# Optimization experiments

Hardware: AMD Instinct MI355X
Metric: run time of the kernel (lower is better)

The kernel has to match this reference:

```python
import jax, jax.numpy as jnp
import numpy as np

MIN_NORM = 1e-15
C = 1.0  # c_in == c_out == 1.0  (K = 1/c)
N, D = 16384, 64


def _expmap0(u, c):
    # exp map at origin of the hyperboloid; u has first coord 0 (tangent at origin)
    sqrtK = (1.0 / c) ** 0.5
    x = u[..., 1:]
    xn = jnp.maximum(jnp.linalg.norm(x, axis=-1, keepdims=True), MIN_NORM)
    theta = xn / sqrtK
    return jnp.concatenate([sqrtK * jnp.cosh(theta), sqrtK * jnp.sinh(theta) * x / xn], axis=-1)


def _logmap0(x, c):
    sqrtK = (1.0 / c) ** 0.5
    y = x[..., 1:]
    yn = jnp.maximum(jnp.linalg.norm(y, axis=-1, keepdims=True), MIN_NORM)
    theta = jnp.maximum(x[..., :1] / sqrtK, 1.0 + 1e-7)
    return jnp.concatenate([jnp.zeros_like(theta), sqrtK * jnp.arccosh(theta) * y / yn], axis=-1)


def _proj(x, c):
    # re-project onto the hyperboloid: recompute the time coordinate
    K = 1.0 / c
    y = x[..., 1:]
    first = jnp.sqrt(jnp.maximum(K + jnp.sum(y * y, axis=-1, keepdims=True), MIN_NORM))
    return jnp.concatenate([first, y], axis=-1)


def setup_inputs():
    key = jax.random.key(0)
    k1, k2, k3 = jax.random.split(key, 3)
    # valid hyperboloid points: expmap0 of tangent vectors (first coord 0)
    tang = 0.5 * jax.random.normal(k1, (N, D - 1), dtype=jnp.float32)
    x = _expmap0(jnp.concatenate([jnp.zeros((N, 1), jnp.float32), tang], axis=-1), C)
    # sparse-ish row-normalized adjacency (avg degree ~32), stored dense
    a = jax.random.uniform(k2, (N, N), dtype=jnp.float32)
    mask = (a > 1.0 - 32.0 / N).astype(jnp.float32)
    adj = mask / jnp.maximum(mask.sum(axis=-1, keepdims=True), 1.0)
    W = (jax.random.normal(k3, (D, D), dtype=jnp.float32) / np.float32(np.sqrt(D)))
    return {"x": x, "adj": adj, "W": W}


def reference(x, adj, W):
    # LorentzLinear (no bias, dropout=0): mobius_matvec = expmap0(logmap0(x) @ W^T)
    u = _logmap0(x, C)                       # [N, D], u[:, 0] == 0
    h = _proj(_expmap0(u @ W.T, C), C)
    # LorentzAgg (no attention): aggregate neighbors in tangent space at origin
    ht = _logmap0(h, C)                      # [N, D]
    h = _proj(_expmap0(adj @ ht, C), C)      # [N, D]
    # LorentzAct: apply act in tangent space at origin, proj_tan0, re-project
    xt = jax.nn.relu(_logmap0(h, C))
    xt = xt * jnp.concatenate([jnp.zeros((1,), xt.dtype), jnp.ones((D - 1,), xt.dtype)])  # proj_tan0
    return _proj(_expmap0(xt, C), C)
```

## Files before the change

### kernel.cpp

```cpp
#include <hip/hip_runtime.h>
#include <math.h>

#define NROWS 16384
#define MINN 1e-15f

typedef float vf4 __attribute__((ext_vector_type(4)));

__device__ __forceinline__ float waveSum(float v) {
    #pragma unroll
    for (int m = 32; m >= 1; m >>= 1) v += __shfl_xor(v, m, 64);
    return v;
}

__global__ __launch_bounds__(256) void prep_kernel(
    const float* __restrict__ x, const float* __restrict__ W,
    float* __restrict__ ht)
{
    __shared__ float WT[64 * 64];
    for (int t = threadIdx.x; t < 64 * 64; t += 256) {
        int k = t >> 6, d = t & 63;
        WT[d * 64 + k] = W[t];
    }
    __syncthreads();
    const int lane = threadIdx.x & 63;
    const int row = blockIdx.x * 4 + (threadIdx.x >> 6);

    float xv = x[row * 64 + lane];
    float sq = (lane == 0) ? 0.f : xv * xv;
    float yn = fmaxf(sqrtf(waveSum(sq)), MINN);
    float theta = fmaxf(__shfl(xv, 0, 64), 1.0f + 1e-7f);
    float s = acoshf(theta) / yn;
    float u = (lane == 0) ? 0.f : s * xv;

    float h1 = 0.f;
    #pragma unroll
    for (int d = 1; d < 64; ++d)
        h1 = fmaf(__shfl(u, d, 64), WT[d * 64 + lane], h1);

    float z = (lane == 0) ? 0.f : h1;
    float zn = fmaxf(sqrtf(waveSum(z * z)), MINN);
    float sh = sinhf(zn);
    float ey = sh * z / zn;
    float s2 = waveSum(ey * ey);
    float first = sqrtf(fmaxf(1.f + s2, MINN));
    float ynb = fmaxf(sqrtf(s2), MINN);
    float th2 = fmaxf(first, 1.0f + 1e-7f);
    float coef = acoshf(th2) / ynb;
    float htv = (lane == 0) ? 0.f : coef * ey;
    ht[row * 64 + lane] = htv;
}

__global__ __launch_bounds__(256) void agg_kernel(
    const float* __restrict__ adj, const float* __restrict__ ht,
    float* __restrict__ out)
{
    const int lane = threadIdx.x & 63;
    const int row = blockIdx.x * 4 + (threadIdx.x >> 6);
    const float* arow = adj + (size_t)row * NROWS;

    float acc = 0.f;
    for (int it = 0; it < NROWS / 1024; ++it) {
        const float* base = arow + it * 1024 + lane * 4;
        vf4 v0 = __builtin_nontemporal_load((const vf4*)(base + 0));
        vf4 v1 = __builtin_nontemporal_load((const vf4*)(base + 256));
        vf4 v2 = __builtin_nontemporal_load((const vf4*)(base + 512));
        vf4 v3 = __builtin_nontemporal_load((const vf4*)(base + 768));
        #pragma unroll
        for (int w = 0; w < 4; ++w) {
            vf4 v = (w == 0) ? v0 : (w == 1) ? v1 : (w == 2) ? v2 : v3;
            unsigned int any = __float_as_uint(v.x) | __float_as_uint(v.y) |
                               __float_as_uint(v.z) | __float_as_uint(v.w);
            unsigned long long mask = __ballot(any != 0u);
            int jwin = it * 1024 + w * 256;
            while (mask) {
                int L = __ffsll((long long)mask) - 1;
                mask &= mask - 1;
                float a0 = __shfl(v.x, L, 64);
                float a1 = __shfl(v.y, L, 64);
                float a2 = __shfl(v.z, L, 64);
                float a3 = __shfl(v.w, L, 64);
                int jbase = jwin + L * 4;
                if (a0 != 0.f) acc = fmaf(a0, ht[(size_t)(jbase + 0) * 64 + lane], acc);
                if (a1 != 0.f) acc = fmaf(a1, ht[(size_t)(jbase + 1) * 64 + lane], acc);
                if (a2 != 0.f) acc = fmaf(a2, ht[(size_t)(jbase + 2) * 64 + lane], acc);
                if (a3 != 0.f) acc = fmaf(a3, ht[(size_t)(jbase + 3) * 64 + lane], acc);
            }
        }
    }

    float z = (lane == 0) ? 0.f : acc;
    float zn = fmaxf(sqrtf(waveSum(z * z)), MINN);
    float sh = sinhf(zn);
    float ey = sh * z / zn;
    float s2 = waveSum(ey * ey);
    float first = sqrtf(fmaxf(1.f + s2, MINN));
    float ynb = fmaxf(sqrtf(s2), MINN);
    float th2 = fmaxf(first, 1.0f + 1e-7f);
    float l = acoshf(th2) / ynb * ey;
    float xt = fmaxf(l, 0.f);
    if (lane == 0) xt = 0.f;
    float xn = fmaxf(sqrtf(waveSum(xt * xt)), MINN);
    float sh2 = sinhf(xn);
    float oy = sh2 * xt / xn;
    float o0 = sqrtf(fmaxf(1.f + waveSum(oy * oy), MINN));
    float outv = (lane == 0) ? o0 : oy;
    out[row * 64 + lane] = outv;
}

extern "C" void kernel_launch(void* const* d_in, const int* in_sizes, int n_in,
                              void* d_out, int out_size, void* d_ws, size_t ws_size,
                              hipStream_t stream) {
    const float* x   = (const float*)d_in[0];
    const float* adj = (const float*)d_in[1];
    const float* W   = (const float*)d_in[2];
    float* out = (float*)d_out;
    float* ht  = (float*)d_ws;

    prep_kernel<<<NROWS / 4, 256, 0, stream>>>(x, W, ht);
    agg_kernel<<<NROWS / 4, 256, 0, stream>>>(adj, ht, out);
}
```

Baseline: 1.344 ms.

## Fuse prep into aggregation by recomputing neighbor ht on the fly

Merges the two kernels into one. Each wave now recomputes the tangent vector (logmap, a 64x64 matvec from shared memory, expmap, proj, logmap) for every nonzero neighbor instead of reading a precomputed ht buffer. It also double-buffers the adjacency loads by prefetching the next 1024-column chunk. This removes a kernel launch and the ht round trip through memory, but it redoes the per-row transform about 32 times per row (the average degree), adding a lot of ALU and shuffle work inside a serial loop.

Result: slower. 1.980 ms (+47.3%).

```diff
diff --git a/kernel.cpp b/kernel.cpp
--- a/kernel.cpp
+++ b/kernel.cpp
@@ -3,6 +3,7 @@
 
 #define NROWS 16384
 #define MINN 1e-15f
+#define NITER (NROWS / 1024)
 
 typedef float vf4 __attribute__((ext_vector_type(4)));
 
@@ -12,20 +13,10 @@
     return v;
 }
 
-__global__ __launch_bounds__(256) void prep_kernel(
-    const float* __restrict__ x, const float* __restrict__ W,
-    float* __restrict__ ht)
+__device__ __forceinline__ float compute_ht(
+    const float* __restrict__ x, const float* WT, int j, int lane)
 {
-    __shared__ float WT[64 * 64];
-    for (int t = threadIdx.x; t < 64 * 64; t += 256) {
-        int k = t >> 6, d = t & 63;
-        WT[d * 64 + k] = W[t];
-    }
-    __syncthreads();
-    const int lane = threadIdx.x & 63;
-    const int row = blockIdx.x * 4 + (threadIdx.x >> 6);
-
-    float xv = x[row * 64 + lane];
+    float xv = x[(size_t)j * 64 + lane];
     float sq = (lane == 0) ? 0.f : xv * xv;
     float yn = fmaxf(sqrtf(waveSum(sq)), MINN);
     float theta = fmaxf(__shfl(xv, 0, 64), 1.0f + 1e-7f);
@@ -46,28 +37,44 @@
     float ynb = fmaxf(sqrtf(s2), MINN);
     float th2 = fmaxf(first, 1.0f + 1e-7f);
     float coef = acoshf(th2) / ynb;
-    float htv = (lane == 0) ? 0.f : coef * ey;
-    ht[row * 64 + lane] = htv;
+    return (lane == 0) ? 0.f : coef * ey;
 }
 
-__global__ __launch_bounds__(256) void agg_kernel(
-    const float* __restrict__ adj, const float* __restrict__ ht,
-    float* __restrict__ out)
+__global__ __launch_bounds__(256) void fused_kernel(
+    const float* __restrict__ x, const float* __restrict__ adj,
+    const float* __restrict__ W, float* __restrict__ out)
 {
     const int lane = threadIdx.x & 63;
     const int row = blockIdx.x * 4 + (threadIdx.x >> 6);
     const float* arow = adj + (size_t)row * NROWS;
 
+    const float* b0 = arow + lane * 4;
+    vf4 c0 = __builtin_nontemporal_load((const vf4*)(b0 + 0));
+    vf4 c1 = __builtin_nontemporal_load((const vf4*)(b0 + 256));
+    vf4 c2 = __builtin_nontemporal_load((const vf4*)(b0 + 512));
+    vf4 c3 = __builtin_nontemporal_load((const vf4*)(b0 + 768));
+
+    __shared__ float WT[64 * 64];
+    for (int t = threadIdx.x; t < 64 * 64; t += 256) {
+        int k = t >> 6, d = t & 63;
+        WT[d * 64 + k] = W[t];
+    }
+    __syncthreads();
+
     float acc = 0.f;
-    for (int it = 0; it < NROWS / 1024; ++it) {
-        const float* base = arow + it * 1024 + lane * 4;
-        vf4 v0 = __builtin_nontemporal_load((const vf4*)(base + 0));
-        vf4 v1 = __builtin_nontemporal_load((const vf4*)(base + 256));
-        vf4 v2 = __builtin_nontemporal_load((const vf4*)(base + 512));
-        vf4 v3 = __builtin_nontemporal_load((const vf4*)(base + 768));
+    for (int it = 0; it < NITER; ++it) {
+        vf4 n0, n1, n2, n3;
+        const bool more = (it + 1 < NITER);
+        if (more) {
+            const float* nb = arow + (size_t)(it + 1) * 1024 + lane * 4;
+            n0 = __builtin_nontemporal_load((const vf4*)(nb + 0));
+            n1 = __builtin_nontemporal_load((const vf4*)(nb + 256));
+            n2 = __builtin_nontemporal_load((const vf4*)(nb + 512));
+            n3 = __builtin_nontemporal_load((const vf4*)(nb + 768));
+        }
         #pragma unroll
         for (int w = 0; w < 4; ++w) {
-            vf4 v = (w == 0) ? v0 : (w == 1) ? v1 : (w == 2) ? v2 : v3;
+            vf4 v = (w == 0) ? c0 : (w == 1) ? c1 : (w == 2) ? c2 : c3;
             unsigned int any = __float_as_uint(v.x) | __float_as_uint(v.y) |
                                __float_as_uint(v.z) | __float_as_uint(v.w);
             unsigned long long mask = __ballot(any != 0u);
@@ -80,12 +87,15 @@
                 float a2 = __shfl(v.z, L, 64);
                 float a3 = __shfl(v.w, L, 64);
                 int jbase = jwin + L * 4;
-                if (a0 != 0.f) acc = fmaf(a0, ht[(size_t)(jbase + 0) * 64 + lane], acc);
-                if (a1 != 0.f) acc = fmaf(a1, ht[(size_t)(jbase + 1) * 64 + lane], acc);
-                if (a2 != 0.f) acc = fmaf(a2, ht[(size_t)(jbase + 2) * 64 + lane], acc);
-                if (a3 != 0.f) acc = fmaf(a3, ht[(size_t)(jbase + 3) * 64 + lane], acc);
+                #pragma unroll 1
+                for (int q = 0; q < 4; ++q) {
+                    float aq = (q == 0) ? a0 : (q == 1) ? a1 : (q == 2) ? a2 : a3;
+                    if (aq != 0.f)
+                        acc = fmaf(aq, compute_ht(x, WT, jbase + q, lane), acc);
+                }
             }
         }
+        if (more) { c0 = n0; c1 = n1; c2 = n2; c3 = n3; }
     }
 
     float z = (lane == 0) ? 0.f : acc;
@@ -114,8 +124,7 @@
     const float* adj = (const float*)d_in[1];
     const float* W   = (const float*)d_in[2];
     float* out = (float*)d_out;
-    float* ht  = (float*)d_ws;
+    (void)d_ws; (void)ws_size;
 
-    prep_kernel<<<NROWS / 4, 256, 0, stream>>>(x, W, ht);
-    agg_kernel<<<NROWS / 4, 256, 0, stream>>>(adj, ht, out);
+    fused_kernel<<<NROWS / 4, 256, 0, stream>>>(x, adj, W, out);
 }
```
